# Performance work log

Measured on AMD Instinct MI355X. Metric: run time of the kernel, lower is better.

Reference implementation:

```python
import jax, jax.numpy as jnp
import numpy as np

NEG = -1e9  # finite mask value (avoids NaN rows for fully-masked queries)


def setup_inputs() -> dict:
    key = jax.random.key(0)
    kq, kk, kv, ks = jax.random.split(key, 4)
    B, H, N, E = 4, 8, 2048, 64
    Q = jax.random.normal(kq, (B, H, N, E), dtype=jnp.float32)
    K = jax.random.normal(kk, (B, H, N, E), dtype=jnp.float32)
    V = jax.random.normal(kv, (B, H, N, E), dtype=jnp.float32)
    seqlens = jax.random.randint(ks, (B,), 1, N + 1, dtype=jnp.int32)
    return {"Q": Q, "K": K, "V": V, "seqlens": seqlens}


def reference(Q, K, V, seqlens):
    # SparTA SeqlenDynamicSparseAttention: per-batch masked attention.
    # scores = Q @ K^T (no 1/sqrt(E) scaling inside the kernel; Q/K are
    # assumed to be already-projected), softmax over keys < seqlen[b],
    # output zeroed for query rows >= seqlen[b].
    B, H, N, E = Q.shape
    pos = jnp.arange(N)
    valid = pos[None, :] < seqlens[:, None]  # [B, N] bool
    scores = jnp.einsum('bhqe,bhke->bhqk', Q, K)  # [B,H,N,N]
    scores = jnp.where(valid[:, None, None, :], scores, NEG)
    probs = jax.nn.softmax(scores, axis=-1)
    out = jnp.einsum('bhqk,bhke->bhqe', probs, V)  # [B,H,N,E]
    out = jnp.where(valid[:, None, :, None], out, 0.0)
    return out
```

## Files before the change

### kernel.cpp

```cpp
#include <hip/hip_runtime.h>

using f32x4 = __attribute__((ext_vector_type(4))) float;
using h16x4 = __attribute__((ext_vector_type(4))) _Float16;
using h16x8 = __attribute__((ext_vector_type(8))) _Float16;

#define NEGBIG (-1e30f)

__launch_bounds__(256)
__global__ void attn_kernel(const float* __restrict__ Qg,
                            const float* __restrict__ Kg,
                            const float* __restrict__ Vg,
                            const int*   __restrict__ seqlens,
                            float*       __restrict__ Og)
{
    constexpr int N = 2048, E = 64;
    const int qblk = blockIdx.x;
    const int bh   = blockIdx.y;
    const int b    = bh >> 3;
    const int seqlen = seqlens[b];
    const int qstart = qblk * 64;
    const int tid = threadIdx.x;

    float* Ob = Og + ((size_t)bh * N + qstart) * E;

    if (qstart >= seqlen) {
        f32x4 z = {0.f, 0.f, 0.f, 0.f};
        f32x4* op = (f32x4*)Ob;
        #pragma unroll
        for (int i = 0; i < 4; ++i) op[tid + i * 256] = z;
        return;
    }

    const float* Qb = Qg + (size_t)bh * N * E;
    const float* Kb = Kg + (size_t)bh * N * E;
    const float* Vb = Vg + (size_t)bh * N * E;

    __shared__ __attribute__((aligned(16))) _Float16 Ksh[64 * 64];
    __shared__ __attribute__((aligned(16))) _Float16 Vsh[64 * 64];

    const int wid  = tid >> 6;
    const int lane = tid & 63;
    const int lg   = lane >> 4;
    const int l16  = lane & 15;

    const int qrow = qstart + wid * 16 + l16;
    h16x8 Qf[2];
    #pragma unroll
    for (int es = 0; es < 2; ++es) {
        const f32x4* qp = (const f32x4*)(Qb + (size_t)qrow * E + es * 32 + lg * 8);
        f32x4 x = qp[0], y = qp[1];
        h16x8 h;
        h[0]=(_Float16)x[0]; h[1]=(_Float16)x[1]; h[2]=(_Float16)x[2]; h[3]=(_Float16)x[3];
        h[4]=(_Float16)y[0]; h[5]=(_Float16)y[1]; h[6]=(_Float16)y[2]; h[7]=(_Float16)y[3];
        Qf[es] = h;
    }

    float m = NEGBIG, L = 0.f;
    f32x4 Ot[4] = {{0,0,0,0},{0,0,0,0},{0,0,0,0},{0,0,0,0}};

    const int vkey    = tid & 63;
    const int ve0base = (tid >> 6) * 8;

    for (int kstart = 0; kstart < seqlen; kstart += 64) {
        __syncthreads();

        #pragma unroll
        for (int it = 0; it < 2; ++it) {
            int cid = tid + it * 256;
            int r = cid >> 3, c = cid & 7;
            const f32x4* gp = (const f32x4*)(Kb + (size_t)(kstart + r) * E + c * 8);
            f32x4 x = gp[0], y = gp[1];
            h16x8 h;
            h[0]=(_Float16)x[0]; h[1]=(_Float16)x[1]; h[2]=(_Float16)x[2]; h[3]=(_Float16)x[3];
            h[4]=(_Float16)y[0]; h[5]=(_Float16)y[1]; h[6]=(_Float16)y[2]; h[7]=(_Float16)y[3];
            *(h16x8*)&Ksh[r * 64 + ((c ^ (r & 7)) << 3)] = h;
        }
        #pragma unroll
        for (int p = 0; p < 2; ++p) {
            int e0 = ve0base + p * 32;
            const f32x4* gp = (const f32x4*)(Vb + (size_t)(kstart + vkey) * E + e0);
            f32x4 x = gp[0], y = gp[1];
            float vv[8] = {x[0], x[1], x[2], x[3], y[0], y[1], y[2], y[3]};
            #pragma unroll
            for (int i = 0; i < 8; ++i) {
                int e = e0 + i;
                Vsh[e * 64 + (((vkey >> 2) ^ ((e & 7) << 1)) << 2) + (vkey & 3)] =
                    (_Float16)vv[i];
            }
        }
        __syncthreads();

        f32x4 St[4];
        #pragma unroll
        for (int kt = 0; kt < 4; ++kt) {
            f32x4 acc = {0, 0, 0, 0};
            int key = kt * 16 + l16;
            #pragma unroll
            for (int es = 0; es < 2; ++es) {
                int c = es * 4 + lg;
                h16x8 kf = *(const h16x8*)&Ksh[key * 64 + ((c ^ (key & 7)) << 3)];
                acc = __builtin_amdgcn_mfma_f32_16x16x32_f16(kf, Qf[es], acc, 0, 0, 0);
            }
            St[kt] = acc;
        }
        if (kstart + 64 > seqlen) {
            #pragma unroll
            for (int kt = 0; kt < 4; ++kt) {
                int kbase = kstart + kt * 16 + lg * 4;
                #pragma unroll
                for (int j = 0; j < 4; ++j)
                    if (kbase + j >= seqlen) St[kt][j] = NEGBIG;
            }
        }

        float tm = NEGBIG;
        #pragma unroll
        for (int kt = 0; kt < 4; ++kt)
            #pragma unroll
            for (int j = 0; j < 4; ++j) tm = fmaxf(tm, St[kt][j]);
        tm = fmaxf(tm, __shfl_xor(tm, 16));
        tm = fmaxf(tm, __shfl_xor(tm, 32));

        float mn = fmaxf(m, tm);
        float scale = __expf(m - mn);
        m = mn;

        float ps = 0.f;
        h16x4 Pf[4];
        #pragma unroll
        for (int kt = 0; kt < 4; ++kt) {
            #pragma unroll
            for (int j = 0; j < 4; ++j) {
                float pv = __expf(St[kt][j] - mn);
                ps += pv;
                Pf[kt][j] = (_Float16)pv;
            }
        }
        ps += __shfl_xor(ps, 16);
        ps += __shfl_xor(ps, 32);
        L = L * scale + ps;

        #pragma unroll
        for (int et = 0; et < 4; ++et) Ot[et] *= scale;

        #pragma unroll
        for (int kt = 0; kt < 4; ++kt) {
            #pragma unroll
            for (int et = 0; et < 4; ++et) {
                int e  = et * 16 + l16;
                int c8 = kt * 4 + lg;
                h16x4 vf = *(const h16x4*)&Vsh[e * 64 + ((c8 ^ ((e & 7) << 1)) << 2)];
                Ot[et] = __builtin_amdgcn_mfma_f32_16x16x16f16(vf, Pf[kt], Ot[et], 0, 0, 0);
            }
        }
    }

    float invL = 1.f / L;
    float* orow = Ob + (size_t)(wid * 16 + l16) * E;
    if (qrow < seqlen) {
        #pragma unroll
        for (int et = 0; et < 4; ++et) {
            f32x4 o = Ot[et] * invL;
            *(f32x4*)(orow + et * 16 + lg * 4) = o;
        }
    } else {
        f32x4 z = {0, 0, 0, 0};
        #pragma unroll
        for (int et = 0; et < 4; ++et)
            *(f32x4*)(orow + et * 16 + lg * 4) = z;
    }
}

extern "C" void kernel_launch(void* const* d_in, const int* in_sizes, int n_in,
                              void* d_out, int out_size, void* d_ws, size_t ws_size,
                              hipStream_t stream)
{
    const float* Q = (const float*)d_in[0];
    const float* K = (const float*)d_in[1];
    const float* V = (const float*)d_in[2];
    const int*   S = (const int*)d_in[3];
    float*       O = (float*)d_out;

    dim3 grid(2048 / 64, 4 * 8);
    attn_kernel<<<grid, 256, 0, stream>>>(Q, K, V, S, O);
}
```

Measured before the change: 142.5 us.

## Double-buffer K/V loads, widen blocks to 128 queries, use exp2 and lazy rescale

Each block now handles 128 query rows with 512 threads, so one staged K/V tile in shared memory is reused by twice as many queries. Global loads for the next K/V tile are issued into registers before computing the current tile, overlapping memory latency with MFMA work. Softmax switches to exp2 with Q pre-scaled by log2e, and the running-max rescale is skipped unless the max grows by more than a threshold. Conversions use packed round-toward-zero fp16 instructions. Risks include higher register pressure, fewer resident blocks, and reduced precision from RTZ conversion and the deferred rescale.

Result: faster. 131.9 us (-7.4%).

```diff
diff --git a/kernel.cpp b/kernel.cpp
--- a/kernel.cpp
+++ b/kernel.cpp
@@ -1,12 +1,24 @@
 #include <hip/hip_runtime.h>
 
-using f32x4 = __attribute__((ext_vector_type(4))) float;
-using h16x4 = __attribute__((ext_vector_type(4))) _Float16;
-using h16x8 = __attribute__((ext_vector_type(8))) _Float16;
+using f32x4  = __attribute__((ext_vector_type(4))) float;
+using h16x2  = __attribute__((ext_vector_type(2))) _Float16;
+using h16x4  = __attribute__((ext_vector_type(4))) _Float16;
+using h16x8  = __attribute__((ext_vector_type(8))) _Float16;
+using fp16x2 = __attribute__((ext_vector_type(2))) __fp16;
 
 #define NEGBIG (-1e30f)
-
-__launch_bounds__(256)
+#define LOG2E  1.44269504f
+
+__device__ inline h16x8 cvt8(f32x4 x, f32x4 y) {
+    union { h16x8 v; fp16x2 p[4]; } u;
+    u.p[0] = __builtin_amdgcn_cvt_pkrtz(x[0], x[1]);
+    u.p[1] = __builtin_amdgcn_cvt_pkrtz(x[2], x[3]);
+    u.p[2] = __builtin_amdgcn_cvt_pkrtz(y[0], y[1]);
+    u.p[3] = __builtin_amdgcn_cvt_pkrtz(y[2], y[3]);
+    return u.v;
+}
+
+__launch_bounds__(512)
 __global__ void attn_kernel(const float* __restrict__ Qg,
                             const float* __restrict__ Kg,
                             const float* __restrict__ Vg,
@@ -18,7 +30,7 @@
     const int bh   = blockIdx.y;
     const int b    = bh >> 3;
     const int seqlen = seqlens[b];
-    const int qstart = qblk * 64;
+    const int qstart = qblk * 128;
     const int tid = threadIdx.x;
 
     float* Ob = Og + ((size_t)bh * N + qstart) * E;
@@ -27,7 +39,7 @@
         f32x4 z = {0.f, 0.f, 0.f, 0.f};
         f32x4* op = (f32x4*)Ob;
         #pragma unroll
-        for (int i = 0; i < 4; ++i) op[tid + i * 256] = z;
+        for (int i = 0; i < 4; ++i) op[tid + i * 512] = z;
         return;
     }
 
@@ -39,57 +51,52 @@
     __shared__ __attribute__((aligned(16))) _Float16 Vsh[64 * 64];
 
     const int wid  = tid >> 6;
+    const int qsub = wid >> 2;
+    const int widq = wid & 3;
     const int lane = tid & 63;
     const int lg   = lane >> 4;
     const int l16  = lane & 15;
 
-    const int qrow = qstart + wid * 16 + l16;
+    const bool active = (qstart + qsub * 64) < seqlen;
+
+    const int qrow = qstart + qsub * 64 + widq * 16 + l16;
     h16x8 Qf[2];
     #pragma unroll
     for (int es = 0; es < 2; ++es) {
         const f32x4* qp = (const f32x4*)(Qb + (size_t)qrow * E + es * 32 + lg * 8);
-        f32x4 x = qp[0], y = qp[1];
-        h16x8 h;
-        h[0]=(_Float16)x[0]; h[1]=(_Float16)x[1]; h[2]=(_Float16)x[2]; h[3]=(_Float16)x[3];
-        h[4]=(_Float16)y[0]; h[5]=(_Float16)y[1]; h[6]=(_Float16)y[2]; h[7]=(_Float16)y[3];
-        Qf[es] = h;
-    }
+        f32x4 x = qp[0] * LOG2E, y = qp[1] * LOG2E;
+        Qf[es] = cvt8(x, y);
+    }
+
+    const int rK  = tid >> 3;
+    const int cK  = tid & 7;
+    const int vkey = tid & 63;
+    const int ve0  = (tid >> 6) * 8;
 
     float m = NEGBIG, L = 0.f;
     f32x4 Ot[4] = {{0,0,0,0},{0,0,0,0},{0,0,0,0},{0,0,0,0}};
 
-    const int vkey    = tid & 63;
-    const int ve0base = (tid >> 6) * 8;
-
-    for (int kstart = 0; kstart < seqlen; kstart += 64) {
-        __syncthreads();
-
-        #pragma unroll
-        for (int it = 0; it < 2; ++it) {
-            int cid = tid + it * 256;
-            int r = cid >> 3, c = cid & 7;
-            const f32x4* gp = (const f32x4*)(Kb + (size_t)(kstart + r) * E + c * 8);
-            f32x4 x = gp[0], y = gp[1];
-            h16x8 h;
-            h[0]=(_Float16)x[0]; h[1]=(_Float16)x[1]; h[2]=(_Float16)x[2]; h[3]=(_Float16)x[3];
-            h[4]=(_Float16)y[0]; h[5]=(_Float16)y[1]; h[6]=(_Float16)y[2]; h[7]=(_Float16)y[3];
-            *(h16x8*)&Ksh[r * 64 + ((c ^ (r & 7)) << 3)] = h;
-        }
-        #pragma unroll
-        for (int p = 0; p < 2; ++p) {
-            int e0 = ve0base + p * 32;
-            const f32x4* gp = (const f32x4*)(Vb + (size_t)(kstart + vkey) * E + e0);
-            f32x4 x = gp[0], y = gp[1];
-            float vv[8] = {x[0], x[1], x[2], x[3], y[0], y[1], y[2], y[3]};
-            #pragma unroll
-            for (int i = 0; i < 8; ++i) {
-                int e = e0 + i;
-                Vsh[e * 64 + (((vkey >> 2) ^ ((e & 7) << 1)) << 2) + (vkey & 3)] =
-                    (_Float16)vv[i];
-            }
-        }
-        __syncthreads();
-
+    auto loadStage = [&](int ks, f32x4& k0, f32x4& k1, f32x4& v0, f32x4& v1) {
+        const f32x4* kp = (const f32x4*)(Kb + (size_t)(ks + rK) * E + cK * 8);
+        k0 = kp[0]; k1 = kp[1];
+        const f32x4* vp = (const f32x4*)(Vb + (size_t)(ks + vkey) * E + ve0);
+        v0 = vp[0]; v1 = vp[1];
+    };
+
+    auto writeStage = [&](const f32x4& k0, const f32x4& k1,
+                          const f32x4& v0, const f32x4& v1) {
+        *(h16x8*)&Ksh[rK * 64 + ((cK ^ (rK & 7)) << 3)] = cvt8(k0, k1);
+        float vv[8] = {v0[0], v0[1], v0[2], v0[3], v1[0], v1[1], v1[2], v1[3]};
+        #pragma unroll
+        for (int i = 0; i < 8; ++i) {
+            int e = ve0 + i;
+            Vsh[e * 64 + (((vkey >> 2) ^ (i << 1)) << 2) + (vkey & 3)] =
+                (_Float16)vv[i];
+        }
+    };
+
+    auto computeTile = [&](int ks) {
+        if (!active) return;
         f32x4 St[4];
         #pragma unroll
         for (int kt = 0; kt < 4; ++kt) {
@@ -103,16 +110,15 @@
             }
             St[kt] = acc;
         }
-        if (kstart + 64 > seqlen) {
+        if (ks + 64 > seqlen) {
             #pragma unroll
             for (int kt = 0; kt < 4; ++kt) {
-                int kbase = kstart + kt * 16 + lg * 4;
+                int kb0 = ks + kt * 16 + lg * 4;
                 #pragma unroll
                 for (int j = 0; j < 4; ++j)
-                    if (kbase + j >= seqlen) St[kt][j] = NEGBIG;
+                    if (kb0 + j >= seqlen) St[kt][j] = NEGBIG;
             }
         }
-
         float tm = NEGBIG;
         #pragma unroll
         for (int kt = 0; kt < 4; ++kt)
@@ -121,27 +127,32 @@
         tm = fmaxf(tm, __shfl_xor(tm, 16));
         tm = fmaxf(tm, __shfl_xor(tm, 32));
 
-        float mn = fmaxf(m, tm);
-        float scale = __expf(m - mn);
-        m = mn;
+        if (__any(tm > m + 8.f)) {
+            float mn = fmaxf(m, tm);
+            float sc = __builtin_amdgcn_exp2f(m - mn);
+            m = mn;
+            L *= sc;
+            #pragma unroll
+            for (int et = 0; et < 4; ++et) Ot[et] *= sc;
+        }
 
         float ps = 0.f;
         h16x4 Pf[4];
         #pragma unroll
         for (int kt = 0; kt < 4; ++kt) {
-            #pragma unroll
-            for (int j = 0; j < 4; ++j) {
-                float pv = __expf(St[kt][j] - mn);
-                ps += pv;
-                Pf[kt][j] = (_Float16)pv;
-            }
+            float p0 = __builtin_amdgcn_exp2f(St[kt][0] - m);
+            float p1 = __builtin_amdgcn_exp2f(St[kt][1] - m);
+            float p2 = __builtin_amdgcn_exp2f(St[kt][2] - m);
+            float p3 = __builtin_amdgcn_exp2f(St[kt][3] - m);
+            ps += (p0 + p1) + (p2 + p3);
+            union { h16x4 v; fp16x2 p[2]; } u;
+            u.p[0] = __builtin_amdgcn_cvt_pkrtz(p0, p1);
+            u.p[1] = __builtin_amdgcn_cvt_pkrtz(p2, p3);
+            Pf[kt] = u.v;
         }
         ps += __shfl_xor(ps, 16);
         ps += __shfl_xor(ps, 32);
-        L = L * scale + ps;
-
-        #pragma unroll
-        for (int et = 0; et < 4; ++et) Ot[et] *= scale;
+        L += ps;
 
         #pragma unroll
         for (int kt = 0; kt < 4; ++kt) {
@@ -153,10 +164,31 @@
                 Ot[et] = __builtin_amdgcn_mfma_f32_16x16x16f16(vf, Pf[kt], Ot[et], 0, 0, 0);
             }
         }
+    };
+
+    f32x4 kA0, kA1, vA0, vA1, kB0, kB1, vB0, vB1;
+    loadStage(0, kA0, kA1, vA0, vA1);
+    int ks = 0;
+    while (true) {
+        __syncthreads();
+        writeStage(kA0, kA1, vA0, vA1);
+        if (ks + 64 < seqlen) loadStage(ks + 64, kB0, kB1, vB0, vB1);
+        __syncthreads();
+        computeTile(ks);
+        ks += 64;
+        if (ks >= seqlen) break;
+
+        __syncthreads();
+        writeStage(kB0, kB1, vB0, vB1);
+        if (ks + 64 < seqlen) loadStage(ks + 64, kA0, kA1, vA0, vA1);
+        __syncthreads();
+        computeTile(ks);
+        ks += 64;
+        if (ks >= seqlen) break;
     }
 
     float invL = 1.f / L;
-    float* orow = Ob + (size_t)(wid * 16 + l16) * E;
+    float* orow = Ob + (size_t)(qsub * 64 + widq * 16 + l16) * E;
     if (qrow < seqlen) {
         #pragma unroll
         for (int et = 0; et < 4; ++et) {
@@ -181,6 +213,6 @@
     const int*   S = (const int*)d_in[3];
     float*       O = (float*)d_out;
 
-    dim3 grid(2048 / 64, 4 * 8);
-    attn_kernel<<<grid, 256, 0, stream>>>(Q, K, V, S, O);
+    dim3 grid(2048 / 128, 4 * 8);
+    attn_kernel<<<grid, 512, 0, stream>>>(Q, K, V, S, O);
 }
```
